# Kernel tuning notes

Hardware: AMD Instinct MI355X
Metric: run time of the kernel (lower is better)

The kernel has to match this reference:

```python
import jax, jax.numpy as jnp
import numpy as np

EMBED_DIM = 512
NUM_HEADS = 8
HEAD_DIM = EMBED_DIM // NUM_HEADS


def setup_inputs() -> dict:
    key = jax.random.key(0)
    k1, k2, k3, k4, k5, k6 = jax.random.split(key, 6)
    B, S, D = 2, 4096, EMBED_DIM
    scale = 1.0 / np.sqrt(D)
    return {
        "inputs": jax.random.normal(k1, (B, S, D), dtype=jnp.float32),
        "Wq": jax.random.normal(k2, (D, D), dtype=jnp.float32) * scale,
        "Wk": jax.random.normal(k3, (D, D), dtype=jnp.float32) * scale,
        "Wv": jax.random.normal(k4, (D, D), dtype=jnp.float32) * scale,
        "Wc": jax.random.normal(k5, (D, D), dtype=jnp.float32) * scale,
        "bc": jax.random.normal(k6, (D,), dtype=jnp.float32) * 0.01,
    }


def reference(inputs, Wq, Wk, Wv, Wc, bc):
    B, S, D = inputs.shape
    H, Hd = NUM_HEADS, HEAD_DIM

    def split_heads(x):
        # [B,S,D] -> [B,H,S,Hd]
        return x.reshape(B, S, H, Hd).transpose(0, 2, 1, 3)

    # nn.Linear applies x @ W.T
    q = split_heads(inputs @ Wq.T).astype(jnp.float32)
    k = split_heads(inputs @ Wk.T).astype(jnp.float32)
    v = split_heads(inputs @ Wv.T).astype(jnp.float32)

    scores = jnp.einsum("bhqd,bhkd->bhqk", q, k) / np.sqrt(Hd).astype(jnp.float32)
    weights = jax.nn.softmax(scores, axis=-1)
    attended = jnp.einsum("bhqk,bhkd->bhqd", weights, v).astype(inputs.dtype)
    attended = attended.transpose(0, 2, 1, 3).reshape(B, S, D)
    return attended @ Wc.T + bc
```

## Files before the change

kernel.cpp:

```cpp
#include <hip/hip_runtime.h>
#include <cstdint>
#include <cstddef>

typedef _Float16 half_t;
typedef half_t h8 __attribute__((ext_vector_type(8)));
typedef half_t h4 __attribute__((ext_vector_type(4)));
typedef float f4 __attribute__((ext_vector_type(4)));
typedef unsigned int u32;

static constexpr int S_LEN  = 4096;
static constexpr int DMODEL = 512;
static constexpr int NH     = 8;
static constexpr int HD     = 64;
static constexpr int BATCH  = 2;
static constexpr int MTOK   = BATCH * S_LEN;

#define QSCALE 0.18033688011112043f

__device__ __forceinline__ void g2lds16(const void* g, void* l) {
    __builtin_amdgcn_global_load_lds(
        (const __attribute__((address_space(1))) u32*)(uintptr_t)g,
        (__attribute__((address_space(3))) u32*)(u32)(uintptr_t)l,
        16, 0, 0);
}

__device__ __forceinline__ f4 mfma16(h8 a, h8 b, f4 c) {
    return __builtin_amdgcn_mfma_f32_16x16x32_f16(a, b, c, 0, 0, 0);
}

__global__ void cvt_x(const float* __restrict__ in, half_t* __restrict__ out) {
    int i = (blockIdx.x * 256 + threadIdx.x) * 8;
    const float4* p = (const float4*)(in + i);
    float4 a = p[0], b = p[1];
    h8 h;
    h[0]=(half_t)a.x; h[1]=(half_t)a.y; h[2]=(half_t)a.z; h[3]=(half_t)a.w;
    h[4]=(half_t)b.x; h[5]=(half_t)b.y; h[6]=(half_t)b.z; h[7]=(half_t)b.w;
    *(h8*)(out + i) = h;
}

__global__ void cvt_w(const float* __restrict__ w0, const float* __restrict__ w1,
                      const float* __restrict__ w2, const float* __restrict__ w3,
                      half_t* __restrict__ o0, half_t* __restrict__ o1,
                      half_t* __restrict__ o2, half_t* __restrict__ o3) {
    int y = blockIdx.y;
    const float* in = (y==0) ? w0 : (y==1) ? w1 : (y==2) ? w2 : w3;
    half_t* out     = (y==0) ? o0 : (y==1) ? o1 : (y==2) ? o2 : o3;
    float s = (y==0) ? QSCALE : 1.0f;
    int i = (blockIdx.x * 256 + threadIdx.x) * 8;
    const float4* p = (const float4*)(in + i);
    float4 a = p[0], b = p[1];
    h8 h;
    h[0]=(half_t)(a.x*s); h[1]=(half_t)(a.y*s); h[2]=(half_t)(a.z*s); h[3]=(half_t)(a.w*s);
    h[4]=(half_t)(b.x*s); h[5]=(half_t)(b.y*s); h[6]=(half_t)(b.z*s); h[7]=(half_t)(b.w*s);
    *(h8*)(out + i) = h;
}

__device__ __forceinline__ void gemm_core(const half_t* __restrict__ A,
                                          const half_t* __restrict__ B,
                                          int m0, int n0, int Kdim,
                                          half_t* As, half_t* Bs,
                                          f4 (&acc)[4][4]) {
    const int tid  = threadIdx.x;
    const int lane = tid & 63;
    const int w    = tid >> 6;
    const int quad = lane >> 4;
    const int low  = lane & 15;
    const int wr   = (w >> 1) * 64;
    const int wc   = (w & 1) * 64;

    f4 zero = {0.f, 0.f, 0.f, 0.f};
    #pragma unroll
    for (int i = 0; i < 4; ++i)
        #pragma unroll
        for (int j = 0; j < 4; ++j) acc[i][j] = zero;

    for (int kk = 0; kk < Kdim; kk += 32) {
        __syncthreads();
        #pragma unroll
        for (int it = 0; it < 2; ++it) {
            int c = tid + 256 * it;
            int row = c >> 2, cs = c & 3;
            int gc = cs ^ ((row >> 1) & 3);
            g2lds16(A + (size_t)(m0 + row) * Kdim + kk + gc * 8, As + c * 8);
        }
        #pragma unroll
        for (int it = 0; it < 2; ++it) {
            int c = tid + 256 * it;
            int row = c >> 2, cs = c & 3;
            int gc = cs ^ ((row >> 1) & 3);
            g2lds16(B + (size_t)(n0 + row) * Kdim + kk + gc * 8, Bs + c * 8);
        }
        __syncthreads();

        h8 af[4], bf[4];
        #pragma unroll
        for (int i = 0; i < 4; ++i) {
            int r = wr + i * 16 + low;
            af[i] = *(const h8*)(As + r * 32 + (quad ^ ((r >> 1) & 3)) * 8);
        }
        #pragma unroll
        for (int j = 0; j < 4; ++j) {
            int r = wc + j * 16 + low;
            bf[j] = *(const h8*)(Bs + r * 32 + (quad ^ ((r >> 1) & 3)) * 8);
        }
        #pragma unroll
        for (int i = 0; i < 4; ++i)
            #pragma unroll
            for (int j = 0; j < 4; ++j)
                acc[i][j] = mfma16(af[i], bf[j], acc[i][j]);
    }
}

__global__ __launch_bounds__(256) void gemm_qkv(
    const half_t* __restrict__ X,
    const half_t* __restrict__ Wq, const half_t* __restrict__ Wk,
    half_t* __restrict__ Q, half_t* __restrict__ K) {
    __shared__ half_t As[128 * 32];
    __shared__ half_t Bs[128 * 32];
    const int z = blockIdx.z;
    const half_t* W = (z == 0) ? Wq : Wk;
    half_t* O       = (z == 0) ? Q  : K;

    const int m0 = blockIdx.y * 128;
    const int n0 = blockIdx.x * 128;
    f4 acc[4][4];
    gemm_core(X, W, m0, n0, DMODEL, As, Bs, acc);

    const int lane = threadIdx.x & 63;
    const int w    = threadIdx.x >> 6;
    const int quad = lane >> 4, low = lane & 15;
    const int wr = (w >> 1) * 64, wc = (w & 1) * 64;

    #pragma unroll
    for (int i = 0; i < 4; ++i) {
        int mb = m0 + wr + i * 16 + quad * 4;
        #pragma unroll
        for (int j = 0; j < 4; ++j) {
            int n = n0 + wc + j * 16 + low;
            int h = n >> 6, d = n & 63;
            #pragma unroll
            for (int r = 0; r < 4; ++r) {
                int m = mb + r;
                int b = m >> 12, s = m & 4095;
                size_t idx = (((size_t)(b * NH + h) << 12) + s) * 64 + d;
                O[idx] = (half_t)acc[i][j][r];
            }
        }
    }
}

__global__ __launch_bounds__(256) void gemm_vt(
    const half_t* __restrict__ X, const half_t* __restrict__ Wv,
    half_t* __restrict__ Vt) {
    __shared__ half_t As[128 * 32];
    __shared__ half_t Bs[128 * 32];
    const int m0 = blockIdx.y * 128;
    const int n0 = blockIdx.x * 128;
    f4 acc[4][4];
    gemm_core(Wv, X, m0, n0, DMODEL, As, Bs, acc);

    const int lane = threadIdx.x & 63;
    const int w    = threadIdx.x >> 6;
    const int quad = lane >> 4, low = lane & 15;
    const int wr = (w >> 1) * 64, wc = (w & 1) * 64;

    #pragma unroll
    for (int i = 0; i < 4; ++i) {
        int dgb = m0 + wr + i * 16 + quad * 4;
        #pragma unroll
        for (int j = 0; j < 4; ++j) {
            int tok = n0 + wc + j * 16 + low;
            int b = tok >> 12, s = tok & 4095;
            #pragma unroll
            for (int r = 0; r < 4; ++r) {
                int dg = dgb + r;
                size_t idx = (((size_t)(b * NH + (dg >> 6)) << 18)) + ((dg & 63) << 12) + s;
                Vt[idx] = (half_t)acc[i][j][r];
            }
        }
    }
}

__global__ __launch_bounds__(256) void gemm_out(
    const half_t* __restrict__ A, const half_t* __restrict__ W,
    const float* __restrict__ bias, float* __restrict__ out) {
    __shared__ half_t As[128 * 32];
    __shared__ half_t Bs[128 * 32];
    const int m0 = blockIdx.y * 128;
    const int n0 = blockIdx.x * 128;
    f4 acc[4][4];
    gemm_core(A, W, m0, n0, DMODEL, As, Bs, acc);

    const int lane = threadIdx.x & 63;
    const int w    = threadIdx.x >> 6;
    const int quad = lane >> 4, low = lane & 15;
    const int wr = (w >> 1) * 64, wc = (w & 1) * 64;

    #pragma unroll
    for (int i = 0; i < 4; ++i) {
        int mb = m0 + wr + i * 16 + quad * 4;
        #pragma unroll
        for (int j = 0; j < 4; ++j) {
            int n = n0 + wc + j * 16 + low;
            float bv = bias[n];
            #pragma unroll
            for (int r = 0; r < 4; ++r)
                out[(size_t)(mb + r) * DMODEL + n] = acc[i][j][r] + bv;
        }
    }
}

__global__ __launch_bounds__(256, 2) void flash_attn(
    const half_t* __restrict__ Q,
    const half_t* __restrict__ K,
    const half_t* __restrict__ V,
    half_t* __restrict__ Oa) {
    __shared__ half_t Ks[2][128 * 64];
    __shared__ half_t Vs[2][64 * 128];
    __shared__ half_t Ps[4 * 32 * 32];

    const int tid  = threadIdx.x;
    const int lane = tid & 63;
    const int w    = tid >> 6;
    const int quad = lane >> 4, low = lane & 15;
    const int bh = blockIdx.y;
    const int q0 = blockIdx.x * 128 + w * 32;

    const half_t* Qb = Q + ((size_t)bh << 18);
    const half_t* Kb = K + ((size_t)bh << 18);
    const half_t* Vb = V + ((size_t)bh << 18);

    h8 qf[2][2];
    #pragma unroll
    for (int i = 0; i < 2; ++i)
        #pragma unroll
        for (int ks = 0; ks < 2; ++ks)
            qf[i][ks] = *(const h8*)(Qb + (size_t)(q0 + i * 16 + low) * 64 + ks * 32 + quad * 8);

    f4 Oacc[2][4];
    f4 zero = {0.f, 0.f, 0.f, 0.f};
    #pragma unroll
    for (int i = 0; i < 2; ++i)
        #pragma unroll
        for (int j = 0; j < 4; ++j) Oacc[i][j] = zero;
    float lrun[2] = {0.f, 0.f};

    half_t* Pw = Ps + w * (32 * 32);

    auto stage = [&](int k0, int p) {
        #pragma unroll
        for (int it = 0; it < 4; ++it) {
            int c = tid + 256 * it;
            int key = c >> 3, cs = c & 7;
            int gc = cs ^ (key & 7);
            g2lds16(Kb + (size_t)(k0 + key) * 64 + gc * 8, &Ks[p][c * 8]);
        }
        #pragma unroll
        for (int it = 0; it < 4; ++it) {
            int c = tid + 256 * it;
            int d = c >> 4, cs = c & 15;
            int gc = cs ^ (d & 7);
            g2lds16(Vb + (size_t)d * S_LEN + k0 + gc * 8, &Vs[p][c * 8]);
        }
    };

    stage(0, 0);

    for (int c = 0; c < S_LEN / 128; ++c) {
        __syncthreads();
        if (c + 1 < S_LEN / 128) stage((c + 1) * 128, (c + 1) & 1);

        const half_t* Kc = Ks[c & 1];
        const half_t* Vc = Vs[c & 1];

        f4 sc[2][8];
        #pragma unroll
        for (int nt = 0; nt < 8; ++nt) {
            int key = nt * 16 + low;
            h8 kf0 = *(const h8*)(Kc + key * 64 + ((0 + quad) ^ (key & 7)) * 8);
            h8 kf1 = *(const h8*)(Kc + key * 64 + ((4 + quad) ^ (key & 7)) * 8);
            #pragma unroll
            for (int i = 0; i < 2; ++i) {
                sc[i][nt] = mfma16(kf0, qf[i][0], zero);
                sc[i][nt] = mfma16(kf1, qf[i][1], sc[i][nt]);
            }
        }

        #pragma unroll
        for (int i = 0; i < 2; ++i) {
            float rs = 0.f;
            #pragma unroll
            for (int nt = 0; nt < 8; ++nt)
                #pragma unroll
                for (int r = 0; r < 4; ++r) {
                    float p = __builtin_amdgcn_exp2f(sc[i][nt][r]);
                    sc[i][nt][r] = p;
                    rs += p;
                }
            lrun[i] += rs;
        }

        #pragma unroll
        for (int g = 0; g < 4; ++g) {
            #pragma unroll
            for (int i = 0; i < 2; ++i) {
                int q = i * 16 + low;
                #pragma unroll
                for (int hn = 0; hn < 2; ++hn) {
                    int nt = 2 * g + hn;
                    h4 pk;
                    pk[0] = (half_t)sc[i][nt][0];
                    pk[1] = (half_t)sc[i][nt][1];
                    pk[2] = (half_t)sc[i][nt][2];
                    pk[3] = (half_t)sc[i][nt][3];
                    int cc = (hn * 2 + (quad >> 1)) ^ ((q >> 1) & 3);
                    *(h4*)(Pw + q * 32 + cc * 8 + (quad & 1) * 4) = pk;
                }
            }
            h8 vf[4];
            #pragma unroll
            for (int j = 0; j < 4; ++j) {
                int d = j * 16 + low;
                vf[j] = *(const h8*)(Vc + d * 128 + (((g * 4 + quad)) ^ (d & 7)) * 8);
            }
            h8 pf[2];
            #pragma unroll
            for (int i = 0; i < 2; ++i) {
                int q = i * 16 + low;
                pf[i] = *(const h8*)(Pw + q * 32 + (quad ^ ((q >> 1) & 3)) * 8);
            }
            #pragma unroll
            for (int i = 0; i < 2; ++i)
                #pragma unroll
                for (int j = 0; j < 4; ++j)
                    Oacc[i][j] = mfma16(vf[j], pf[i], Oacc[i][j]);
        }
    }

    #pragma unroll
    for (int i = 0; i < 2; ++i) {
        lrun[i] += __shfl_xor(lrun[i], 16);
        lrun[i] += __shfl_xor(lrun[i], 32);
    }

    const int b = bh >> 3, h = bh & 7;
    #pragma unroll
    for (int i = 0; i < 2; ++i) {
        float inv = 1.0f / lrun[i];
        int qg = q0 + i * 16 + low;
        #pragma unroll
        for (int j = 0; j < 4; ++j) {
            h4 o;
            #pragma unroll
            for (int r = 0; r < 4; ++r) o[r] = (half_t)(Oacc[i][j][r] * inv);
            *(h4*)(Oa + ((size_t)(b * S_LEN + qg)) * DMODEL + h * 64 + j * 16 + quad * 4) = o;
        }
    }
}

extern "C" void kernel_launch(void* const* d_in, const int* in_sizes, int n_in,
                              void* d_out, int out_size, void* d_ws, size_t ws_size,
                              hipStream_t stream) {
    const float* X  = (const float*)d_in[0];
    const float* Wq = (const float*)d_in[1];
    const float* Wk = (const float*)d_in[2];
    const float* Wv = (const float*)d_in[3];
    const float* Wc = (const float*)d_in[4];
    const float* bc = (const float*)d_in[5];
    float* out = (float*)d_out;

    char* ws = (char*)d_ws;
    const size_t SZ_X = (size_t)MTOK * DMODEL * 2;
    const size_t SZ_W = (size_t)DMODEL * DMODEL * 2;
    half_t* Xh   = (half_t*)(ws);
    half_t* Wqh  = (half_t*)(ws + SZ_X);
    half_t* Wkh  = (half_t*)(ws + SZ_X + SZ_W);
    half_t* Wvh  = (half_t*)(ws + SZ_X + 2 * SZ_W);
    half_t* Wch  = (half_t*)(ws + SZ_X + 3 * SZ_W);
    half_t* Qh   = (half_t*)(ws + SZ_X + 4 * SZ_W);
    half_t* Kh   = (half_t*)(ws + 2 * SZ_X + 4 * SZ_W);
    half_t* Vt   = (half_t*)(ws + 3 * SZ_X + 4 * SZ_W);
    half_t* Att  = (half_t*)(ws + 4 * SZ_X + 4 * SZ_W);

    cvt_x<<<2048, 256, 0, stream>>>(X, Xh);
    cvt_w<<<dim3(128, 4), 256, 0, stream>>>(Wq, Wk, Wv, Wc, Wqh, Wkh, Wvh, Wch);
    gemm_qkv<<<dim3(4, 64, 2), 256, 0, stream>>>(Xh, Wqh, Wkh, Qh, Kh);
    gemm_vt<<<dim3(64, 4), 256, 0, stream>>>(Xh, Wvh, Vt);
    flash_attn<<<dim3(32, 16), 256, 0, stream>>>(Qh, Kh, Vt, Att);
    gemm_out<<<dim3(4, 64), 256, 0, stream>>>(Att, Wch, bc, out);
}
```

Baseline: 204.9 us.

## Shrink GEMM tiles to 64x128, merge QKV projections, double-buffer P tiles

The projection and output GEMMs now use 64x128 block tiles instead of 128x128, giving 512 blocks per matrix, with launch bounds raised to allow four blocks per CU. The Q, K and V^T projections are merged into one launch with a z-dimension of three. This is meant to fill more of the GPU's CUs and to remove one kernel launch. In flash attention the per-wave P scratch tile is double-buffered across groups, which could drop an LDS write-after-read hazard between consecutive groups but uses more shared memory. Smaller tiles lower operand reuse per block.

```diff
diff --git a/kernel.cpp b/kernel.cpp
--- a/kernel.cpp
+++ b/kernel.cpp
@@ -55,30 +55,29 @@
     *(h8*)(out + i) = h;
 }
 
-__device__ __forceinline__ void gemm_core(const half_t* __restrict__ A,
-                                          const half_t* __restrict__ B,
-                                          int m0, int n0, int Kdim,
-                                          half_t* As, half_t* Bs,
-                                          f4 (&acc)[4][4]) {
+__device__ __forceinline__ void gemm_core2(const half_t* __restrict__ A,
+                                           const half_t* __restrict__ B,
+                                           int m0, int n0, int Kdim,
+                                           half_t* As, half_t* Bs,
+                                           f4 (&acc)[2][4]) {
     const int tid  = threadIdx.x;
     const int lane = tid & 63;
     const int w    = tid >> 6;
     const int quad = lane >> 4;
     const int low  = lane & 15;
-    const int wr   = (w >> 1) * 64;
+    const int wr   = (w >> 1) * 32;
     const int wc   = (w & 1) * 64;
 
     f4 zero = {0.f, 0.f, 0.f, 0.f};
     #pragma unroll
-    for (int i = 0; i < 4; ++i)
+    for (int i = 0; i < 2; ++i)
         #pragma unroll
         for (int j = 0; j < 4; ++j) acc[i][j] = zero;
 
     for (int kk = 0; kk < Kdim; kk += 32) {
         __syncthreads();
-        #pragma unroll
-        for (int it = 0; it < 2; ++it) {
-            int c = tid + 256 * it;
+        {
+            int c = tid;
             int row = c >> 2, cs = c & 3;
             int gc = cs ^ ((row >> 1) & 3);
             g2lds16(A + (size_t)(m0 + row) * Kdim + kk + gc * 8, As + c * 8);
@@ -92,9 +91,9 @@
         }
         __syncthreads();
 
-        h8 af[4], bf[4];
-        #pragma unroll
-        for (int i = 0; i < 4; ++i) {
+        h8 af[2], bf[4];
+        #pragma unroll
+        for (int i = 0; i < 2; ++i) {
             int r = wr + i * 16 + low;
             af[i] = *(const h8*)(As + r * 32 + (quad ^ ((r >> 1) & 3)) * 8);
         }
@@ -104,100 +103,94 @@
             bf[j] = *(const h8*)(Bs + r * 32 + (quad ^ ((r >> 1) & 3)) * 8);
         }
         #pragma unroll
-        for (int i = 0; i < 4; ++i)
+        for (int i = 0; i < 2; ++i)
             #pragma unroll
             for (int j = 0; j < 4; ++j)
                 acc[i][j] = mfma16(af[i], bf[j], acc[i][j]);
     }
 }
 
-__global__ __launch_bounds__(256) void gemm_qkv(
+__global__ __launch_bounds__(256, 4) void gemm_proj(
     const half_t* __restrict__ X,
-    const half_t* __restrict__ Wq, const half_t* __restrict__ Wk,
-    half_t* __restrict__ Q, half_t* __restrict__ K) {
-    __shared__ half_t As[128 * 32];
+    const half_t* __restrict__ Wq, const half_t* __restrict__ Wk, const half_t* __restrict__ Wv,
+    half_t* __restrict__ Q, half_t* __restrict__ K, half_t* __restrict__ Vt) {
+    __shared__ half_t As[64 * 32];
     __shared__ half_t Bs[128 * 32];
-    const int z = blockIdx.z;
-    const half_t* W = (z == 0) ? Wq : Wk;
-    half_t* O       = (z == 0) ? Q  : K;
-
-    const int m0 = blockIdx.y * 128;
-    const int n0 = blockIdx.x * 128;
-    f4 acc[4][4];
-    gemm_core(X, W, m0, n0, DMODEL, As, Bs, acc);
+    const int z  = blockIdx.z;
+    const int bx = blockIdx.x;
+
+    const half_t *A, *B;
+    int m0, n0;
+    if (z < 2) {
+        A = X; B = (z == 0) ? Wq : Wk;
+        m0 = (bx >> 2) * 64; n0 = (bx & 3) * 128;
+    } else {
+        A = Wv; B = X;
+        m0 = (bx & 7) * 64; n0 = (bx >> 3) * 128;
+    }
+    f4 acc[2][4];
+    gemm_core2(A, B, m0, n0, DMODEL, As, Bs, acc);
 
     const int lane = threadIdx.x & 63;
     const int w    = threadIdx.x >> 6;
     const int quad = lane >> 4, low = lane & 15;
-    const int wr = (w >> 1) * 64, wc = (w & 1) * 64;
-
-    #pragma unroll
-    for (int i = 0; i < 4; ++i) {
-        int mb = m0 + wr + i * 16 + quad * 4;
-        #pragma unroll
-        for (int j = 0; j < 4; ++j) {
-            int n = n0 + wc + j * 16 + low;
-            int h = n >> 6, d = n & 63;
-            #pragma unroll
-            for (int r = 0; r < 4; ++r) {
-                int m = mb + r;
-                int b = m >> 12, s = m & 4095;
-                size_t idx = (((size_t)(b * NH + h) << 12) + s) * 64 + d;
-                O[idx] = (half_t)acc[i][j][r];
-            }
-        }
-    }
-}
-
-__global__ __launch_bounds__(256) void gemm_vt(
-    const half_t* __restrict__ X, const half_t* __restrict__ Wv,
-    half_t* __restrict__ Vt) {
-    __shared__ half_t As[128 * 32];
+    const int wr = (w >> 1) * 32, wc = (w & 1) * 64;
+
+    if (z < 2) {
+        half_t* O = (z == 0) ? Q : K;
+        #pragma unroll
+        for (int i = 0; i < 2; ++i) {
+            int mb = m0 + wr + i * 16 + quad * 4;
+            #pragma unroll
+            for (int j = 0; j < 4; ++j) {
+                int n = n0 + wc + j * 16 + low;
+                int h = n >> 6, d = n & 63;
+                #pragma unroll
+                for (int r = 0; r < 4; ++r) {
+                    int m = mb + r;
+                    int b = m >> 12, s = m & 4095;
+                    size_t idx = (((size_t)(b * NH + h) << 12) + s) * 64 + d;
+                    O[idx] = (half_t)acc[i][j][r];
+                }
+            }
+        }
+    } else {
+        #pragma unroll
+        for (int i = 0; i < 2; ++i) {
+            int dgb = m0 + wr + i * 16 + quad * 4;
+            #pragma unroll
+            for (int j = 0; j < 4; ++j) {
+                int tok = n0 + wc + j * 16 + low;
+                int b = tok >> 12, s = tok & 4095;
+                #pragma unroll
+                for (int r = 0; r < 4; ++r) {
+                    int dg = dgb + r;
+                    size_t idx = (((size_t)(b * NH + (dg >> 6)) << 18)) + ((dg & 63) << 12) + s;
+                    Vt[idx] = (half_t)acc[i][j][r];
+                }
+            }
+        }
+    }
+}
+
+__global__ __launch_bounds__(256, 4) void gemm_out(
+    const half_t* __restrict__ A, const half_t* __restrict__ W,
+    const float* __restrict__ bias, float* __restrict__ out) {
+    __shared__ half_t As[64 * 32];
     __shared__ half_t Bs[128 * 32];
-    const int m0 = blockIdx.y * 128;
-    const int n0 = blockIdx.x * 128;
-    f4 acc[4][4];
-    gemm_core(Wv, X, m0, n0, DMODEL, As, Bs, acc);
+    const int bx = blockIdx.x;
+    const int m0 = (bx >> 2) * 64;
+    const int n0 = (bx & 3) * 128;
+    f4 acc[2][4];
+    gemm_core2(A, W, m0, n0, DMODEL, As, Bs, acc);
 
     const int lane = threadIdx.x & 63;
     const int w    = threadIdx.x >> 6;
     const int quad = lane >> 4, low = lane & 15;
-    const int wr = (w >> 1) * 64, wc = (w & 1) * 64;
-
-    #pragma unroll
-    for (int i = 0; i < 4; ++i) {
-        int dgb = m0 + wr + i * 16 + quad * 4;
-        #pragma unroll
-        for (int j = 0; j < 4; ++j) {
-            int tok = n0 + wc + j * 16 + low;
-            int b = tok >> 12, s = tok & 4095;
-            #pragma unroll
-            for (int r = 0; r < 4; ++r) {
-                int dg = dgb + r;
-                size_t idx = (((size_t)(b * NH + (dg >> 6)) << 18)) + ((dg & 63) << 12) + s;
-                Vt[idx] = (half_t)acc[i][j][r];
-            }
-        }
-    }
-}
-
-__global__ __launch_bounds__(256) void gemm_out(
-    const half_t* __restrict__ A, const half_t* __restrict__ W,
-    const float* __restrict__ bias, float* __restrict__ out) {
-    __shared__ half_t As[128 * 32];
-    __shared__ half_t Bs[128 * 32];
-    const int m0 = blockIdx.y * 128;
-    const int n0 = blockIdx.x * 128;
-    f4 acc[4][4];
-    gemm_core(A, W, m0, n0, DMODEL, As, Bs, acc);
-
-    const int lane = threadIdx.x & 63;
-    const int w    = threadIdx.x >> 6;
-    const int quad = lane >> 4, low = lane & 15;
-    const int wr = (w >> 1) * 64, wc = (w & 1) * 64;
-
-    #pragma unroll
-    for (int i = 0; i < 4; ++i) {
+    const int wr = (w >> 1) * 32, wc = (w & 1) * 64;
+
+    #pragma unroll
+    for (int i = 0; i < 2; ++i) {
         int mb = m0 + wr + i * 16 + quad * 4;
         #pragma unroll
         for (int j = 0; j < 4; ++j) {
@@ -217,7 +210,7 @@
     half_t* __restrict__ Oa) {
     __shared__ half_t Ks[2][128 * 64];
     __shared__ half_t Vs[2][64 * 128];
-    __shared__ half_t Ps[4 * 32 * 32];
+    __shared__ half_t Ps[2][4 * 32 * 32];
 
     const int tid  = threadIdx.x;
     const int lane = tid & 63;
@@ -245,8 +238,6 @@
         for (int j = 0; j < 4; ++j) Oacc[i][j] = zero;
     float lrun[2] = {0.f, 0.f};
 
-    half_t* Pw = Ps + w * (32 * 32);
-
     auto stage = [&](int k0, int p) {
         #pragma unroll
         for (int it = 0; it < 4; ++it) {
@@ -302,6 +293,7 @@
 
         #pragma unroll
         for (int g = 0; g < 4; ++g) {
+            half_t* Pw = &Ps[g & 1][w * (32 * 32)];
             #pragma unroll
             for (int i = 0; i < 2; ++i) {
                 int q = i * 16 + low;
@@ -384,8 +376,7 @@
 
     cvt_x<<<2048, 256, 0, stream>>>(X, Xh);
     cvt_w<<<dim3(128, 4), 256, 0, stream>>>(Wq, Wk, Wv, Wc, Wqh, Wkh, Wvh, Wch);
-    gemm_qkv<<<dim3(4, 64, 2), 256, 0, stream>>>(Xh, Wqh, Wkh, Qh, Kh);
-    gemm_vt<<<dim3(64, 4), 256, 0, stream>>>(Xh, Wvh, Vt);
+    gemm_proj<<<dim3(512, 1, 3), 256, 0, stream>>>(Xh, Wqh, Wkh, Wvh, Qh, Kh, Vt);
     flash_attn<<<dim3(32, 16), 256, 0, stream>>>(Qh, Kh, Vt, Att);
-    gemm_out<<<dim3(4, 64), 256, 0, stream>>>(Att, Wch, bc, out);
-}
+    gemm_out<<<512, 256, 0, stream>>>(Att, Wch, bc, out);
+}
```

Result: no change. 204.8 us (-0.0%).
